# Optimization experiments

Measured on AMD Instinct MI355X. Metric: run time of the kernel, lower is better.

## Reference

```python
import jax, jax.numpy as jnp
import numpy as np

N, E, D, F = 8192, 262144, 256, 512  # nodes, edges, hidden_dim, ffn hidden
M = 256  # performer num_random_features (default)


def _ln(x, g, b, eps=1e-5):
    mu = jnp.mean(x, axis=-1, keepdims=True)
    var = jnp.mean((x - mu) ** 2, axis=-1, keepdims=True)
    return (x - mu) * jax.lax.rsqrt(var + eps) * g + b


def setup_inputs() -> dict:
    key = jax.random.key(0)
    ks = jax.random.split(key, 16)
    s = 1.0 / np.sqrt(D)
    return {
        "h": jax.random.normal(ks[0], (N, D), dtype=jnp.float32),
        "edge_index": jax.random.randint(ks[1], (2, E), 0, N, dtype=jnp.int32),
        "W_gcn": jax.random.normal(ks[2], (D, D), dtype=jnp.float32) * s,
        "b_gcn": jnp.zeros((D,), jnp.float32),
        "Wq": jax.random.normal(ks[3], (D, D), dtype=jnp.float32) * s,
        "bq": jnp.zeros((D,), jnp.float32),
        "Wk": jax.random.normal(ks[4], (D, D), dtype=jnp.float32) * s,
        "bk": jnp.zeros((D,), jnp.float32),
        "Wv": jax.random.normal(ks[5], (D, D), dtype=jnp.float32) * s,
        "bv": jnp.zeros((D,), jnp.float32),
        "Wo": jax.random.normal(ks[6], (D, D), dtype=jnp.float32) * s,
        "bo": jnp.zeros((D,), jnp.float32),
        "RF": jax.random.normal(ks[7], (M, D), dtype=jnp.float32) * s,  # random feature projection
        "g1": jnp.ones((D,), jnp.float32), "be1": jnp.zeros((D,), jnp.float32),
        "g2": jnp.ones((D,), jnp.float32), "be2": jnp.zeros((D,), jnp.float32),
        "g3": jnp.ones((D,), jnp.float32), "be3": jnp.zeros((D,), jnp.float32),
        "W1": jax.random.normal(ks[8], (D, F), dtype=jnp.float32) * s,
        "b1": jnp.zeros((F,), jnp.float32),
        "W2": jax.random.normal(ks[9], (F, D), dtype=jnp.float32) * (1.0 / np.sqrt(F)),
        "b2": jnp.zeros((D,), jnp.float32),
    }


def _gps_forward(h, edge_index, W_gcn, b_gcn, Wq, bq, Wk, bk, Wv, bv, Wo, bo, RF,
                 g1, be1, g2, be2, g3, be3, W1, b1, W2, b2):
    n = h.shape[0]
    # ---- local GCNConv (add self loops, symmetric norm) ----
    loops = jnp.arange(n, dtype=edge_index.dtype)
    src = jnp.concatenate([edge_index[0], loops])
    dst = jnp.concatenate([edge_index[1], loops])
    deg = jax.ops.segment_sum(jnp.ones_like(src, dtype=h.dtype), dst, num_segments=n)
    dinv = jnp.where(deg > 0, jax.lax.rsqrt(jnp.maximum(deg, 1e-12)), 0.0)
    coef = dinv[src] * dinv[dst]  # [E+N]
    xw = h @ W_gcn  # [N, D]
    h_local = jax.ops.segment_sum(xw[src] * coef[:, None], dst, num_segments=n) + b_gcn
    h1 = _ln(h + h_local, g1, be1)  # dropout p applied in train only; eval here
    # ---- global Performer attention (as written: dense NxN in feature space) ----
    q = h1 @ Wq + bq
    k = h1 @ Wk + bk
    v = h1 @ Wv + bv
    qf = q @ RF.T  # [N, M]
    kf = k @ RF.T  # [N, M]
    scores = (qf @ kf.T) / jnp.sqrt(jnp.asarray(h.shape[-1], h.dtype))  # [N, N]
    attw = jax.nn.softmax(scores, axis=-1)
    h_global = (attw @ v) @ Wo + bo
    h2 = _ln(h1 + h_global, g2, be2)
    # ---- FFN ----
    h_ffn = jnp.maximum(h2 @ W1 + b1, 0.0) @ W2 + b2
    return _ln(h2 + h_ffn, g3, be3)


def reference(h, edge_index, W_gcn, b_gcn, Wq, bq, Wk, bk, Wv, bv, Wo, bo, RF,
              g1, be1, g2, be2, g3, be3, W1, b1, W2, b2):
    return _gps_forward(h, edge_index, W_gcn, b_gcn, Wq, bq, Wk, bk, Wv, bv, Wo, bo, RF,
                        g1, be1, g2, be2, g3, be3, W1, b1, W2, b2)
```

## Files before the change

### kernel.cpp

```cpp
#include <hip/hip_runtime.h>
#include <hip/hip_bf16.h>

#define NN 8192
#define EE 262144
#define DD 256
#define FF 512
#define MM 256

typedef __attribute__((ext_vector_type(8))) short short8v;
typedef __attribute__((ext_vector_type(16))) float float16v;

__device__ __forceinline__ ushort f2bf(float x) {
  union { float f; unsigned u; } c; c.f = x;
  unsigned r = (c.u + 0x7FFF + ((c.u >> 16) & 1)) >> 16;
  return (ushort)r;
}
__device__ __forceinline__ float b2f(ushort u) {
  union { unsigned u; float f; } c; c.u = ((unsigned)u) << 16;
  return c.f;
}
__device__ __forceinline__ void async_copy16(void* lds, const void* g) {
  __builtin_amdgcn_global_load_lds(
      (const __attribute__((address_space(1))) void*)g,
      (__attribute__((address_space(3))) void*)lds, 16, 0, 0);
}

__global__ void count_kernel(const int* __restrict__ ei, int* __restrict__ degi) {
  int i = blockIdx.x * blockDim.x + threadIdx.x;
  if (i < EE) atomicAdd(&degi[ei[EE + i]], 1);
}

__global__ __launch_bounds__(1024) void scan_kernel(const int* __restrict__ degi,
                                                    int* __restrict__ csr_off,
                                                    float* __restrict__ dinv) {
  __shared__ int part[1024];
  int tid = threadIdx.x;
  int base = tid * 8;
  int loc[8], dv[8]; int s = 0;
#pragma unroll
  for (int i = 0; i < 8; ++i) { int d = degi[base + i]; dv[i] = d; loc[i] = s; s += d; }
  part[tid] = s;
  __syncthreads();
  for (int off = 1; off < 1024; off <<= 1) {
    int v = (tid >= off) ? part[tid - off] : 0;
    __syncthreads();
    part[tid] += v;
    __syncthreads();
  }
  int pre = (tid == 0) ? 0 : part[tid - 1];
#pragma unroll
  for (int i = 0; i < 8; ++i) {
    csr_off[base + i] = pre + loc[i];
    dinv[base + i] = rsqrtf((float)(dv[i] + 1));
  }
  if (tid == 1023) csr_off[NN] = part[1023];
}

__global__ void fill_kernel(const int* __restrict__ ei, const int* __restrict__ csr_off,
                            int* __restrict__ cursor, int* __restrict__ csr_src) {
  int i = blockIdx.x * blockDim.x + threadIdx.x;
  if (i < EE) {
    int d = ei[EE + i];
    int pos = csr_off[d] + atomicAdd(&cursor[d], 1);
    csr_src[pos] = ei[i];
  }
}

#define QSCALE 0.090168441f
#define P1B 10753
__global__ __launch_bounds__(256) void prep_kernel(
    const float* __restrict__ h, const float* __restrict__ W_gcn,
    const float* __restrict__ Wv, const float* __restrict__ Wo,
    const float* __restrict__ W1, const float* __restrict__ W2,
    const float* __restrict__ bv,
    const float* __restrict__ Wq, const float* __restrict__ Wk,
    const float* __restrict__ bq, const float* __restrict__ bk,
    const float* __restrict__ RF,
    ushort* __restrict__ hb, ushort* __restrict__ WgcnT, ushort* __restrict__ Wcat,
    ushort* __restrict__ WoT, ushort* __restrict__ W1T, ushort* __restrict__ W2T,
    ushort* __restrict__ RFb, ushort* __restrict__ Wqb, ushort* __restrict__ Wkb,
    float* __restrict__ bcat, int* __restrict__ degi, int* __restrict__ cursor)
{
  if (blockIdx.x < P1B) {
    int i = blockIdx.x * 256 + threadIdx.x;
    const int R0 = NN * DD;
    const int R1 = R0 + DD * DD;
    const int R2 = R1 + DD * DD;
    const int R3 = R2 + DD * DD;
    const int R4 = R3 + DD * FF;
    const int R5 = R4 + FF * DD;
    const int R6 = R5 + DD;
    const int R7 = R6 + DD * DD;
    const int R8 = R7 + DD * DD;
    const int R9 = R8 + DD * DD;
    if (i < R0) {
      hb[i] = f2bf(h[i]);
    } else if (i < R1) {
      int j = i - R0; int n = j >> 8, k = j & 255;
      WgcnT[(n << 8) | k] = f2bf(W_gcn[k * DD + n]);
    } else if (i < R2) {
      int j = i - R1; int n = j >> 8, k = j & 255;
      Wcat[((512 + n) << 8) | k] = f2bf(Wv[k * DD + n]);
    } else if (i < R3) {
      int j = i - R2; int n = j >> 8, k = j & 255;
      WoT[(n << 8) | k] = f2bf(Wo[k * DD + n]);
    } else if (i < R4) {
      int j = i - R3; int n = j >> 8, k = j & 255;
      W1T[(n << 8) | k] = f2bf(W1[k * FF + n]);
    } else if (i < R5) {
      int j = i - R4; int n = j >> 9, k = j & 511;
      W2T[n * FF + k] = f2bf(W2[k * DD + n]);
    } else if (i < R6) {
      bcat[512 + (i - R5)] = bv[i - R5];
    } else if (i < R7) {
      int j = i - R6;
      RFb[j] = f2bf(RF[j]);
    } else if (i < R8) {
      int j = i - R7;
      Wqb[j] = f2bf(Wq[j] * QSCALE);
    } else if (i < R9) {
      int j = i - R8;
      Wkb[j] = f2bf(Wk[j]);
    }
  } else if (blockIdx.x < P1B + 2) {
    const int b = blockIdx.x - P1B;
    const int m = threadIdx.x;
    const float* bvec = (b == 0) ? bq : bk;
    const float alpha = (b == 0) ? QSCALE : 1.0f;
    float s = 0.0f;
    for (int j = 0; j < DD; ++j) s = fmaf(bvec[j], RF[m * DD + j], s);
    bcat[(b == 0 ? 0 : 256) + m] = s * alpha;
  } else {
    int i = (blockIdx.x - P1B - 2) * 256 + threadIdx.x;
    if (i < NN) { degi[i] = 0; cursor[i] = 0; }
  }
}

template<int OMODE, bool RELU>
__global__ __launch_bounds__(512) void gemm_bf16_kernel(
    const ushort* __restrict__ A, const ushort* __restrict__ BT,
    const float* __restrict__ bias, void* __restrict__ Cv,
    void* __restrict__ Cv2, void* __restrict__ Cv3,
    int M, int N, int K)
{
  __shared__ ushort As[2][4096];
  __shared__ ushort Bs[2][4096];
  const int tid = threadIdx.x;
  const int c32 = tid & 31, hi = (tid >> 5) & 1;
  const int wv = tid >> 6;
  const int q = wv & 3, ks = wv >> 2;
  const int qm = (q >> 1) << 5, qn = (q & 1) << 5;
  const int m0 = blockIdx.y * 64, n0 = blockIdx.x * 64;

  const int sr = tid >> 3, spsl = tid & 7;
  const int ssl = spsl ^ ((sr >> 2) & 7);
  const ushort* Asrc = A + (size_t)(m0 + sr) * K + (ssl << 3);
  const ushort* Bsrc = BT + (size_t)(n0 + sr) * K + (ssl << 3);

  const int ra = qm + c32, rb = qn + c32;
  const int ga = (ra >> 2) & 7, gb = (rb >> 2) & 7;

  float16v acc = (float16v)(0.0f);

#define GS(b, k0) { \
    async_copy16(&As[b][tid << 3], Asrc + (k0)); \
    async_copy16(&Bs[b][tid << 3], Bsrc + (k0)); }

  GS(0, 0)
  const int nk = K >> 6;
  for (int kt = 0; kt < nk; ++kt) {
    asm volatile("s_waitcnt vmcnt(0)" ::: "memory");
    __syncthreads();
    if (kt + 1 < nk) GS((kt + 1) & 1, (kt + 1) << 6)
    const ushort* as_ = As[kt & 1];
    const ushort* bs_ = Bs[kt & 1];
    __builtin_amdgcn_s_setprio(1);
#pragma unroll
    for (int k2 = 0; k2 < 2; ++k2) {
      const int k16 = (ks << 1) + k2;
      const int sl = (k16 << 1) + hi;
      short8v af = *(const short8v*)&as_[(ra << 6) + ((sl ^ ga) << 3)];
      short8v bf = *(const short8v*)&bs_[(rb << 6) + ((sl ^ gb) << 3)];
      acc = __builtin_amdgcn_mfma_f32_32x32x16_bf16(af, bf, acc, 0, 0, 0);
    }
    __builtin_amdgcn_s_setprio(0);
  }
#undef GS

  __syncthreads();
  float* red = (float*)&As[0][0];
  if (ks == 1) {
#pragma unroll
    for (int r = 0; r < 16; ++r) {
      const int crow = (r & 3) + ((r >> 2) << 3) + (hi << 2);
      red[(q << 10) + (crow << 5) + c32] = acc[r];
    }
  }
  __syncthreads();
  if (ks == 0) {
    const int col = n0 + qn + c32;
    const float bv = bias ? bias[col] : 0.0f;
#pragma unroll
    for (int r = 0; r < 16; ++r) {
      const int crow = (r & 3) + ((r >> 2) << 3) + (hi << 2);
      const int m = m0 + qm + crow;
      float v = acc[r] + red[(q << 10) + (crow << 5) + c32] + bv;
      if (RELU) v = fmaxf(v, 0.0f);
      if (OMODE == 0) {
        ((float*)Cv)[(size_t)m * N + col] = v;
      } else if (OMODE == 4) {
        ((ushort*)Cv)[(size_t)m * N + col] = f2bf(v);
      } else {
        if (col < 256) {
          ((ushort*)Cv)[(size_t)m * 256 + col] = f2bf(v);
        } else if (col < 512) {
          const int c2 = (col - 256) ^ ((m & 7) << 3) ^ (((m >> 3) & 3) << 6);
          ((ushort*)Cv2)[(size_t)m * 256 + c2] = f2bf(v);
        } else {
          ((ushort*)Cv3)[(size_t)(col - 512) * NN + m] = f2bf(v);
        }
      }
    }
  }
}

__global__ __launch_bounds__(256) void gcn_gather_ln_kernel(
    const ushort* __restrict__ xwb, const float* __restrict__ h,
    const float* __restrict__ dinv, const int* __restrict__ csr_off,
    const int* __restrict__ csr_src, const float* __restrict__ b_gcn,
    const float* __restrict__ g1, const float* __restrict__ be1,
    float* __restrict__ h1, ushort* __restrict__ h1b)
{
  const int node = blockIdx.x * 4 + (threadIdx.x >> 6);
  const int t = threadIdx.x & 63;
  const int c4 = t << 2;
  const float di = dinv[node];
  const int e0 = csr_off[node], e1 = csr_off[node + 1];
  float acc[4] = {0.f, 0.f, 0.f, 0.f};
  for (int e = e0; e < e1; ++e) {
    int s = csr_src[e];
    float ds = dinv[s];
    ushort4 xv = *(const ushort4*)&xwb[(size_t)s * DD + c4];
    acc[0] = fmaf(b2f(xv.x), ds, acc[0]);
    acc[1] = fmaf(b2f(xv.y), ds, acc[1]);
    acc[2] = fmaf(b2f(xv.z), ds, acc[2]);
    acc[3] = fmaf(b2f(xv.w), ds, acc[3]);
  }
  ushort4 sv = *(const ushort4*)&xwb[(size_t)node * DD + c4];
  float4 hv = *(const float4*)&h[(size_t)node * DD + c4];
  float4 bg = *(const float4*)&b_gcn[c4];
  const float dii = di * di;
  float y[4];
  y[0] = fmaf(acc[0], di, b2f(sv.x) * dii) + bg.x + hv.x;
  y[1] = fmaf(acc[1], di, b2f(sv.y) * dii) + bg.y + hv.y;
  y[2] = fmaf(acc[2], di, b2f(sv.z) * dii) + bg.z + hv.z;
  y[3] = fmaf(acc[3], di, b2f(sv.w) * dii) + bg.w + hv.w;
  float s1 = (y[0] + y[1]) + (y[2] + y[3]);
  float s2 = (y[0]*y[0] + y[1]*y[1]) + (y[2]*y[2] + y[3]*y[3]);
#pragma unroll
  for (int m = 1; m <= 32; m <<= 1) { s1 += __shfl_xor(s1, m); s2 += __shfl_xor(s2, m); }
  float mu = s1 * (1.0f / 256.0f);
  float var = s2 * (1.0f / 256.0f) - mu * mu;
  float inv = rsqrtf(fmaxf(var, 0.0f) + 1e-5f);
  float4 g4 = *(const float4*)&g1[c4];
  float4 b4 = *(const float4*)&be1[c4];
  float v0 = (y[0] - mu) * inv * g4.x + b4.x;
  float v1 = (y[1] - mu) * inv * g4.y + b4.y;
  float v2 = (y[2] - mu) * inv * g4.z + b4.z;
  float v3 = (y[3] - mu) * inv * g4.w + b4.w;
  *(float4*)&h1[(size_t)node * DD + c4] = make_float4(v0, v1, v2, v3);
  ushort4 ob; ob.x = f2bf(v0); ob.y = f2bf(v1); ob.z = f2bf(v2); ob.w = f2bf(v3);
  *(ushort4*)&h1b[(node << 8) + c4] = ob;
}

__global__ __launch_bounds__(256) void ln_res_kernel(
    const float* __restrict__ a, const float* __restrict__ b,
    const float* __restrict__ g, const float* __restrict__ be,
    float* __restrict__ out, ushort* __restrict__ outb)
{
  const int row = blockIdx.x * 4 + (threadIdx.x >> 6);
  const int t = threadIdx.x & 63;
  const int c4 = t << 2;
  float4 av = *(const float4*)&a[(size_t)row * DD + c4];
  float4 bv = *(const float4*)&b[(size_t)row * DD + c4];
  float y[4] = {av.x + bv.x, av.y + bv.y, av.z + bv.z, av.w + bv.w};
  float s1 = (y[0] + y[1]) + (y[2] + y[3]);
  float s2 = (y[0]*y[0] + y[1]*y[1]) + (y[2]*y[2] + y[3]*y[3]);
#pragma unroll
  for (int m = 1; m <= 32; m <<= 1) { s1 += __shfl_xor(s1, m); s2 += __shfl_xor(s2, m); }
  float mu = s1 * (1.0f / 256.0f);
  float var = s2 * (1.0f / 256.0f) - mu * mu;
  float inv = rsqrtf(fmaxf(var, 0.0f) + 1e-5f);
  float4 g4 = *(const float4*)&g[c4];
  float4 b4 = *(const float4*)&be[c4];
  float v0 = (y[0] - mu) * inv * g4.x + b4.x;
  float v1 = (y[1] - mu) * inv * g4.y + b4.y;
  float v2 = (y[2] - mu) * inv * g4.z + b4.z;
  float v3 = (y[3] - mu) * inv * g4.w + b4.w;
  *(float4*)&out[(size_t)row * DD + c4] = make_float4(v0, v1, v2, v3);
  if (outb) {
    ushort4 ob; ob.x = f2bf(v0); ob.y = f2bf(v1); ob.z = f2bf(v2); ob.w = f2bf(v3);
    *(ushort4*)&outb[(row << 8) + c4] = ob;
  }
}

__global__ __launch_bounds__(256, 2) void flash_mfma_kernel(
    const ushort* __restrict__ qb, const ushort* __restrict__ kb,
    const ushort* __restrict__ vbT, ushort* __restrict__ opb,
    float* __restrict__ ml, int ksn, int kchunk)
{
  __shared__ ushort Kbuf[2][8192];
  __shared__ ushort Vbuf[2][8192];

  const int tid = threadIdx.x;
  const int l = tid & 63, wv = tid >> 6;
  const int c32 = l & 31, hi = l >> 5;
  const int qt = blockIdx.x / ksn, ks = blockIdx.x % ksn;
  const int q0 = qt * 128;
  const int kbase = ks * kchunk;

  const int vrow = tid >> 2;
  const ushort* kptr = kb + (size_t)(kbase + (tid >> 5)) * 256 + ((tid & 31) << 3);
  const ushort* vptr = vbT + (size_t)vrow * NN + kbase + (((tid & 3) ^ ((vrow >> 3) & 3)) << 3);

#define FSTAGE(b) { \
    _Pragma("unroll") \
    for (int c = 0; c < 4; ++c) { \
      async_copy16(&Kbuf[b][((c << 8) + tid) << 3], kptr + (size_t)c * (8 * 256)); \
      async_copy16(&Vbuf[b][((c << 8) + tid) << 3], vptr + (size_t)c * (64 * NN)); \
    } }

  FSTAGE(0)

  short8v qfr[16];
  {
    const ushort* qrow = qb + (size_t)(q0 + wv * 32 + c32) * 256 + (hi << 3);
#pragma unroll
    for (int kk = 0; kk < 16; ++kk)
      qfr[kk] = *(const short8v*)(qrow + (kk << 4));
  }

  float16v acc[8];
#pragma unroll
  for (int dt = 0; dt < 8; ++dt) acc[dt] = (float16v)(0.0f);
  float lsum = 0.f;

  const int ksw = ((c32 & 7) << 3) | (((c32 >> 3) & 3) << 6);
  const int vsw = (c32 >> 3) & 3;
  const int voff0 = (hi ^ vsw) << 3;
  const int voff1 = ((2 + hi) ^ vsw) << 3;

  const int nit = kchunk >> 5;
  for (int it = 0; it < nit; ++it) {
    asm volatile("s_waitcnt vmcnt(0)" ::: "memory");
    __syncthreads();
    if (it + 1 < nit) {
      kptr += 32 * 256;
      vptr += 32;
      FSTAGE((it + 1) & 1)
    }
    const ushort* Kp = Kbuf[it & 1];
    const ushort* Vp = Vbuf[it & 1];

    float16v s = (float16v)(0.0f);
    __builtin_amdgcn_s_setprio(1);
#pragma unroll
    for (int kk = 0; kk < 16; ++kk) {
      short8v kf = *(const short8v*)&Kp[(c32 << 8) + (((kk << 4) + (hi << 3)) ^ ksw)];
      s = __builtin_amdgcn_mfma_f32_32x32x16_bf16(kf, qfr[kk], s, 0, 0, 0);
    }
    __builtin_amdgcn_s_setprio(0);

    float p[16];
#pragma unroll
    for (int r = 0; r < 16; ++r) p[r] = exp2f(s[r]);
    {
      float t0 = (p[0] + p[1]) + (p[2] + p[3]);
      float t1 = (p[4] + p[5]) + (p[6] + p[7]);
      float t2 = (p[8] + p[9]) + (p[10] + p[11]);
      float t3 = (p[12] + p[13]) + (p[14] + p[15]);
      lsum += (t0 + t1) + (t2 + t3);
    }
    unsigned u0, u1, u2, u3, u4, u5, u6, u7;
    asm("v_cvt_pk_bf16_f32 %0, %1, %2" : "=v"(u0) : "v"(p[0]),  "v"(p[1]));
    asm("v_cvt_pk_bf16_f32 %0, %1, %2" : "=v"(u1) : "v"(p[2]),  "v"(p[3]));
    asm("v_cvt_pk_bf16_f32 %0, %1, %2" : "=v"(u2) : "v"(p[4]),  "v"(p[5]));
    asm("v_cvt_pk_bf16_f32 %0, %1, %2" : "=v"(u3) : "v"(p[6]),  "v"(p[7]));
    asm("v_cvt_pk_bf16_f32 %0, %1, %2" : "=v"(u4) : "v"(p[8]),  "v"(p[9]));
    asm("v_cvt_pk_bf16_f32 %0, %1, %2" : "=v"(u5) : "v"(p[10]), "v"(p[11]));
    asm("v_cvt_pk_bf16_f32 %0, %1, %2" : "=v"(u6) : "v"(p[12]), "v"(p[13]));
    asm("v_cvt_pk_bf16_f32 %0, %1, %2" : "=v"(u7) : "v"(p[14]), "v"(p[15]));
    asm volatile("v_permlane32_swap_b32 %0, %1" : "+v"(u0), "+v"(u2));
    asm volatile("v_permlane32_swap_b32 %0, %1" : "+v"(u1), "+v"(u3));
    asm volatile("v_permlane32_swap_b32 %0, %1" : "+v"(u4), "+v"(u6));
    asm volatile("v_permlane32_swap_b32 %0, %1" : "+v"(u5), "+v"(u7));
    union { unsigned uu[4]; short8v v; } P0, P1;
    P0.uu[0] = u0; P0.uu[1] = u1; P0.uu[2] = u2; P0.uu[3] = u3;
    P1.uu[0] = u4; P1.uu[1] = u5; P1.uu[2] = u6; P1.uu[3] = u7;

    __builtin_amdgcn_s_setprio(1);
#pragma unroll
    for (int dt = 0; dt < 8; ++dt) {
      const int drow = (dt << 5) + c32;
      short8v vf0 = *(const short8v*)&Vp[(drow << 5) + voff0];
      short8v vf1 = *(const short8v*)&Vp[(drow << 5) + voff1];
      acc[dt] = __builtin_amdgcn_mfma_f32_32x32x16_bf16(P0.v, vf0, acc[dt], 0, 0, 0);
      acc[dt] = __builtin_amdgcn_mfma_f32_32x32x16_bf16(P1.v, vf1, acc[dt], 0, 0, 0);
    }
    __builtin_amdgcn_s_setprio(0);
  }
#undef FSTAGE

  float lt = lsum + __shfl_xor(lsum, 32);
  if (hi == 0) ml[(size_t)ks * NN + q0 + wv * 32 + c32] = lt;
  ushort* op = opb + (size_t)ks * (NN * DD);
#pragma unroll
  for (int dt = 0; dt < 8; ++dt)
#pragma unroll
    for (int r = 0; r < 16; ++r) {
      const int qrow = q0 + wv * 32 + (r & 3) + ((r >> 2) << 3) + (hi << 2);
      op[(size_t)qrow * DD + (dt << 5) + c32] = f2bf(acc[dt][r]);
    }
}

__global__ __launch_bounds__(256) void flash_merge_kernel(
    const ushort* __restrict__ opb, const float* __restrict__ ml,
    ushort* __restrict__ hgb, int ksn)
{
  const int t = threadIdx.x;
  const int row = blockIdx.x * 8 + (t >> 5);
  const int cg = t & 31;
  float num[8] = {0.f, 0.f, 0.f, 0.f, 0.f, 0.f, 0.f, 0.f};
  float L = 0.f;
  for (int i = 0; i < ksn; ++i) {
    L += ml[(size_t)i * NN + row];
    short8v v = *(const short8v*)&opb[(size_t)i * NN * DD + (size_t)row * DD + (cg << 3)];
#pragma unroll
    for (int j = 0; j < 8; ++j) num[j] += b2f((ushort)v[j]);
  }
  float inv = 1.0f / L;
  short8v o;
#pragma unroll
  for (int j = 0; j < 8; ++j) o[j] = (short)f2bf(num[j] * inv);
  *(short8v*)&hgb[(row << 8) + (cg << 3)] = o;
}

extern "C" void kernel_launch(void* const* d_in, const int* in_sizes, int n_in,
                              void* d_out, int out_size, void* d_ws, size_t ws_size,
                              hipStream_t stream) {
  (void)in_sizes; (void)n_in; (void)out_size;
  const float* h     = (const float*)d_in[0];
  const int*   ei    = (const int*)  d_in[1];
  const float* W_gcn = (const float*)d_in[2];
  const float* b_gcn = (const float*)d_in[3];
  const float* Wq    = (const float*)d_in[4];
  const float* bq    = (const float*)d_in[5];
  const float* Wk    = (const float*)d_in[6];
  const float* bk    = (const float*)d_in[7];
  const float* Wv    = (const float*)d_in[8];
  const float* bv    = (const float*)d_in[9];
  const float* Wo    = (const float*)d_in[10];
  const float* bo    = (const float*)d_in[11];
  const float* RF    = (const float*)d_in[12];
  const float* g1    = (const float*)d_in[13];
  const float* be1   = (const float*)d_in[14];
  const float* g2    = (const float*)d_in[15];
  const float* be2   = (const float*)d_in[16];
  const float* g3    = (const float*)d_in[17];
  const float* be3   = (const float*)d_in[18];
  const float* W1    = (const float*)d_in[19];
  const float* b1    = (const float*)d_in[20];
  const float* W2    = (const float*)d_in[21];
  const float* b2    = (const float*)d_in[22];
  float* out = (float*)d_out;

  const size_t M2 = (size_t)NN * DD;
  const int ksn = (ws_size >= (size_t)64 * 1024 * 1024) ? 8 : 4;
  const int kchunk = NN / ksn;

  char* base = (char*)d_ws;
  float*  h1   = (float*)base;  base += M2 * 4;
  ushort* hbX  = (ushort*)base; base += M2 * 2;
  ushort* h1bX = (ushort*)base; base += M2 * 2;
  ushort* qb   = (ushort*)base; base += M2 * 2;
  ushort* kb   = (ushort*)base; base += M2 * 2;
  ushort* vbT  = (ushort*)base; base += M2 * 2;
  ushort* opb  = (ushort*)base;
  float*  R    = (float*)opb;   base += (size_t)ksn * M2 * 2;
  float*  mlf  = (float*)base;  base += (size_t)8 * NN * 4;
  ushort* WgcnT = (ushort*)base; base += DD * DD * 2;
  ushort* Wcat  = (ushort*)base; base += (size_t)768 * DD * 2;
  ushort* WoT   = (ushort*)base; base += DD * DD * 2;
  ushort* W1T   = (ushort*)base; base += FF * DD * 2;
  ushort* W2T   = (ushort*)base; base += DD * FF * 2;
  ushort* RFb   = (ushort*)base; base += DD * DD * 2;
  ushort* Wqb   = (ushort*)base; base += DD * DD * 2;
  ushort* Wkb   = (ushort*)base; base += DD * DD * 2;
  float*  bcat  = (float*)base;  base += 768 * 4;
  float*  dinv  = (float*)base;  base += NN * 4;
  int* degi    = (int*)base; base += NN * 4;
  int* cursor  = (int*)base; base += NN * 4;
  int* csr_off = (int*)base; base += (NN + 4) * 4;
  int* csr_src = (int*)base; base += EE * 4;

  ushort* xwb = (ushort*)R;
  float*  hgo = R;
  float*  h2  = R + M2;
  ushort* tb  = qb;
  float*  f2  = h1;
  ushort* hgb = hbX;
  ushort* h2b = h1bX;

  prep_kernel<<<P1B + 2 + 32, 256, 0, stream>>>(
      h, W_gcn, Wv, Wo, W1, W2, bv, Wq, Wk, bq, bk, RF,
      hbX, WgcnT, Wcat, WoT, W1T, W2T, RFb, Wqb, Wkb, bcat, degi, cursor);

  gemm_bf16_kernel<4, false><<<dim3(4, 4), 512, 0, stream>>>(
      RFb, Wqb, nullptr, Wcat, nullptr, nullptr, DD, DD, DD);
  gemm_bf16_kernel<4, false><<<dim3(4, 4), 512, 0, stream>>>(
      RFb, Wkb, nullptr, Wcat + 256 * 256, nullptr, nullptr, DD, DD, DD);

  count_kernel<<<EE / 256, 256, 0, stream>>>(ei, degi);
  scan_kernel<<<1, 1024, 0, stream>>>(degi, csr_off, dinv);
  fill_kernel<<<EE / 256, 256, 0, stream>>>(ei, csr_off, cursor, csr_src);

  gemm_bf16_kernel<4, false><<<dim3(DD / 64, NN / 64), 512, 0, stream>>>(
      hbX, WgcnT, nullptr, xwb, nullptr, nullptr, NN, DD, DD);
  gcn_gather_ln_kernel<<<NN / 4, 256, 0, stream>>>(xwb, h, dinv, csr_off, csr_src, b_gcn, g1, be1, h1, h1bX);
  gemm_bf16_kernel<3, false><<<dim3(768 / 64, NN / 64), 512, 0, stream>>>(
      h1bX, Wcat, bcat, qb, kb, vbT, NN, 768, DD);
  flash_mfma_kernel<<<(NN / 128) * ksn, 256, 0, stream>>>(qb, kb, vbT, opb, mlf, ksn, kchunk);
  flash_merge_kernel<<<NN / 8, 256, 0, stream>>>(opb, mlf, hgb, ksn);
  gemm_bf16_kernel<0, false><<<dim3(DD / 64, NN / 64), 512, 0, stream>>>(
      hgb, WoT, bo, hgo, nullptr, nullptr, NN, DD, DD);
  ln_res_kernel<<<NN / 4, 256, 0, stream>>>(h1, hgo, g2, be2, h2, h2b);
  gemm_bf16_kernel<4, true ><<<dim3(FF / 64, NN / 64), 512, 0, stream>>>(
      h2b, W1T, b1, tb, nullptr, nullptr, NN, FF, DD);
  gemm_bf16_kernel<0, false><<<dim3(DD / 64, NN / 64), 512, 0, stream>>>(
      tb, W2T, b2, f2, nullptr, nullptr, NN, DD, FF);
  ln_res_kernel<<<NN / 4, 256, 0, stream>>>(h2, f2, g3, be3, out, nullptr);
}
```

Baseline: 225.9 us.

## Fuse output projection, LayerNorms and FFN into one epilogue kernel; merge prep launches

Replaces the Wo GEMM, two residual LayerNorm kernels and both FFN GEMMs with a single per-32-row kernel that keeps h2 and the ReLU intermediate in LDS. This removes several global round trips of NxD and NxF activations and four launches. It also folds the degree counting into prep_kernel, merges the two RF·Wq/Wk GEMMs into one launch, and vectorises the transposed V store. The cost is that the fused kernel uses a lot of LDS per block and reads weights directly from global memory without staging them.

After: 215.6 us. 1.05x faster.

```diff
diff --git a/kernel.cpp b/kernel.cpp
--- a/kernel.cpp
+++ b/kernel.cpp
@@ -23,11 +23,6 @@
   __builtin_amdgcn_global_load_lds(
       (const __attribute__((address_space(1))) void*)g,
       (__attribute__((address_space(3))) void*)lds, 16, 0, 0);
-}
-
-__global__ void count_kernel(const int* __restrict__ ei, int* __restrict__ degi) {
-  int i = blockIdx.x * blockDim.x + threadIdx.x;
-  if (i < EE) atomicAdd(&degi[ei[EE + i]], 1);
 }
 
 __global__ __launch_bounds__(1024) void scan_kernel(const int* __restrict__ degi,
@@ -75,11 +70,11 @@
     const float* __restrict__ bv,
     const float* __restrict__ Wq, const float* __restrict__ Wk,
     const float* __restrict__ bq, const float* __restrict__ bk,
-    const float* __restrict__ RF,
+    const float* __restrict__ RF, const int* __restrict__ ei,
     ushort* __restrict__ hb, ushort* __restrict__ WgcnT, ushort* __restrict__ Wcat,
     ushort* __restrict__ WoT, ushort* __restrict__ W1T, ushort* __restrict__ W2T,
-    ushort* __restrict__ RFb, ushort* __restrict__ Wqb, ushort* __restrict__ Wkb,
-    float* __restrict__ bcat, int* __restrict__ degi, int* __restrict__ cursor)
+    ushort* __restrict__ RFb, ushort* __restrict__ Wqkb,
+    float* __restrict__ bcat, int* __restrict__ degi)
 {
   if (blockIdx.x < P1B) {
     int i = blockIdx.x * 256 + threadIdx.x;
@@ -117,10 +112,10 @@
       RFb[j] = f2bf(RF[j]);
     } else if (i < R8) {
       int j = i - R7;
-      Wqb[j] = f2bf(Wq[j] * QSCALE);
+      Wqkb[j] = f2bf(Wq[j] * QSCALE);
     } else if (i < R9) {
       int j = i - R8;
-      Wkb[j] = f2bf(Wk[j]);
+      Wqkb[DD * DD + j] = f2bf(Wk[j]);
     }
   } else if (blockIdx.x < P1B + 2) {
     const int b = blockIdx.x - P1B;
@@ -132,7 +127,7 @@
     bcat[(b == 0 ? 0 : 256) + m] = s * alpha;
   } else {
     int i = (blockIdx.x - P1B - 2) * 256 + threadIdx.x;
-    if (i < NN) { degi[i] = 0; cursor[i] = 0; }
+    if (i < EE) atomicAdd(&degi[ei[EE + i]], 1);
   }
 }
 
@@ -200,24 +195,35 @@
   if (ks == 0) {
     const int col = n0 + qn + c32;
     const float bv = bias ? bias[col] : 0.0f;
-#pragma unroll
-    for (int r = 0; r < 16; ++r) {
-      const int crow = (r & 3) + ((r >> 2) << 3) + (hi << 2);
-      const int m = m0 + qm + crow;
-      float v = acc[r] + red[(q << 10) + (crow << 5) + c32] + bv;
-      if (RELU) v = fmaxf(v, 0.0f);
-      if (OMODE == 0) {
-        ((float*)Cv)[(size_t)m * N + col] = v;
-      } else if (OMODE == 4) {
-        ((ushort*)Cv)[(size_t)m * N + col] = f2bf(v);
-      } else {
-        if (col < 256) {
-          ((ushort*)Cv)[(size_t)m * 256 + col] = f2bf(v);
-        } else if (col < 512) {
-          const int c2 = (col - 256) ^ ((m & 7) << 3) ^ (((m >> 3) & 3) << 6);
-          ((ushort*)Cv2)[(size_t)m * 256 + c2] = f2bf(v);
+    if (OMODE == 3 && col >= 512) {
+#pragma unroll
+      for (int g = 0; g < 4; ++g) {
+        float v0 = acc[g * 4 + 0] + red[(q << 10) + (((0) + (g << 3) + (hi << 2)) << 5) + c32] + bv;
+        float v1 = acc[g * 4 + 1] + red[(q << 10) + (((1) + (g << 3) + (hi << 2)) << 5) + c32] + bv;
+        float v2 = acc[g * 4 + 2] + red[(q << 10) + (((2) + (g << 3) + (hi << 2)) << 5) + c32] + bv;
+        float v3 = acc[g * 4 + 3] + red[(q << 10) + (((3) + (g << 3) + (hi << 2)) << 5) + c32] + bv;
+        ushort4 o; o.x = f2bf(v0); o.y = f2bf(v1); o.z = f2bf(v2); o.w = f2bf(v3);
+        *(ushort4*)&((ushort*)Cv3)[(size_t)(col - 512) * NN + m0 + qm + (g << 3) + (hi << 2)] = o;
+      }
+    } else {
+#pragma unroll
+      for (int r = 0; r < 16; ++r) {
+        const int crow = (r & 3) + ((r >> 2) << 3) + (hi << 2);
+        const int m = m0 + qm + crow;
+        float v = acc[r] + red[(q << 10) + (crow << 5) + c32] + bv;
+        if (RELU) v = fmaxf(v, 0.0f);
+        if (OMODE == 4) {
+          ((ushort*)Cv)[(size_t)m * N + col] = f2bf(v);
+        } else if (OMODE == 5) {
+          if (col < 256) ((ushort*)Cv)[(size_t)m * 256 + col] = f2bf(v);
+          else ((ushort*)Cv)[(size_t)(256 + m) * 256 + (col - 256)] = f2bf(v);
         } else {
-          ((ushort*)Cv3)[(size_t)(col - 512) * NN + m] = f2bf(v);
+          if (col < 256) {
+            ((ushort*)Cv)[(size_t)m * 256 + col] = f2bf(v);
+          } else {
+            const int c2 = (col - 256) ^ ((m & 7) << 3) ^ (((m >> 3) & 3) << 6);
+            ((ushort*)Cv2)[(size_t)m * 256 + c2] = f2bf(v);
+          }
         }
       }
     }
@@ -273,37 +279,6 @@
   *(ushort4*)&h1b[(node << 8) + c4] = ob;
 }
 
-__global__ __launch_bounds__(256) void ln_res_kernel(
-    const float* __restrict__ a, const float* __restrict__ b,
-    const float* __restrict__ g, const float* __restrict__ be,
-    float* __restrict__ out, ushort* __restrict__ outb)
-{
-  const int row = blockIdx.x * 4 + (threadIdx.x >> 6);
-  const int t = threadIdx.x & 63;
-  const int c4 = t << 2;
-  float4 av = *(const float4*)&a[(size_t)row * DD + c4];
-  float4 bv = *(const float4*)&b[(size_t)row * DD + c4];
-  float y[4] = {av.x + bv.x, av.y + bv.y, av.z + bv.z, av.w + bv.w};
-  float s1 = (y[0] + y[1]) + (y[2] + y[3]);
-  float s2 = (y[0]*y[0] + y[1]*y[1]) + (y[2]*y[2] + y[3]*y[3]);
-#pragma unroll
-  for (int m = 1; m <= 32; m <<= 1) { s1 += __shfl_xor(s1, m); s2 += __shfl_xor(s2, m); }
-  float mu = s1 * (1.0f / 256.0f);
-  float var = s2 * (1.0f / 256.0f) - mu * mu;
-  float inv = rsqrtf(fmaxf(var, 0.0f) + 1e-5f);
-  float4 g4 = *(const float4*)&g[c4];
-  float4 b4 = *(const float4*)&be[c4];
-  float v0 = (y[0] - mu) * inv * g4.x + b4.x;
-  float v1 = (y[1] - mu) * inv * g4.y + b4.y;
-  float v2 = (y[2] - mu) * inv * g4.z + b4.z;
-  float v3 = (y[3] - mu) * inv * g4.w + b4.w;
-  *(float4*)&out[(size_t)row * DD + c4] = make_float4(v0, v1, v2, v3);
-  if (outb) {
-    ushort4 ob; ob.x = f2bf(v0); ob.y = f2bf(v1); ob.z = f2bf(v2); ob.w = f2bf(v3);
-    *(ushort4*)&outb[(row << 8) + c4] = ob;
-  }
-}
-
 __global__ __launch_bounds__(256, 2) void flash_mfma_kernel(
     const ushort* __restrict__ qb, const ushort* __restrict__ kb,
     const ushort* __restrict__ vbT, ushort* __restrict__ opb,
@@ -443,6 +418,146 @@
 #pragma unroll
   for (int j = 0; j < 8; ++j) o[j] = (short)f2bf(num[j] * inv);
   *(short8v*)&hgb[(row << 8) + (cg << 3)] = o;
+}
+
+__global__ __launch_bounds__(512, 4) void epilogue_kernel(
+    const ushort* __restrict__ hgb, const float* __restrict__ h1,
+    const ushort* __restrict__ WoT, const float* __restrict__ bo,
+    const float* __restrict__ g2, const float* __restrict__ be2,
+    const ushort* __restrict__ W1T, const float* __restrict__ b1,
+    const ushort* __restrict__ W2T, const float* __restrict__ b2,
+    const float* __restrict__ g3, const float* __restrict__ be3,
+    float* __restrict__ out)
+{
+  __shared__ float  yL[32 * 256];
+  __shared__ ushort h2bL[32 * 256];
+  __shared__ ushort tL[32 * 512];
+
+  const int tid = threadIdx.x;
+  const int c32 = tid & 31, hi = (tid >> 5) & 1;
+  const int wv = tid >> 6;
+  const int lane = tid & 63;
+  const int m0 = blockIdx.x * 32;
+  const int n0 = wv << 5;
+  const int col = n0 + c32;
+
+  float16v acc = (float16v)(0.0f);
+#pragma unroll
+  for (int k0 = 0; k0 < 256; k0 += 16) {
+    short8v af = *(const short8v*)&hgb[(size_t)(m0 + c32) * 256 + k0 + (hi << 3)];
+    short8v bf = *(const short8v*)&WoT[(size_t)col * 256 + k0 + (hi << 3)];
+    acc = __builtin_amdgcn_mfma_f32_32x32x16_bf16(af, bf, acc, 0, 0, 0);
+  }
+  {
+    const float bov = bo[col];
+#pragma unroll
+    for (int r = 0; r < 16; ++r) {
+      const int row = (r & 3) + ((r >> 2) << 3) + (hi << 2);
+      yL[(row << 8) + col] = acc[r] + bov + h1[(size_t)(m0 + row) * 256 + col];
+    }
+  }
+  __syncthreads();
+#pragma unroll
+  for (int rr = 0; rr < 4; ++rr) {
+    const int row = (wv << 2) + rr;
+    const int c4 = lane << 2;
+    float4 v = *(const float4*)&yL[(row << 8) + c4];
+    float s1 = (v.x + v.y) + (v.z + v.w);
+    float s2 = (v.x * v.x + v.y * v.y) + (v.z * v.z + v.w * v.w);
+#pragma unroll
+    for (int m = 1; m <= 32; m <<= 1) { s1 += __shfl_xor(s1, m); s2 += __shfl_xor(s2, m); }
+    float mu = s1 * (1.0f / 256.0f);
+    float var = s2 * (1.0f / 256.0f) - mu * mu;
+    float inv = rsqrtf(fmaxf(var, 0.0f) + 1e-5f);
+    float4 g4 = *(const float4*)&g2[c4];
+    float4 b4 = *(const float4*)&be2[c4];
+    float o0 = (v.x - mu) * inv * g4.x + b4.x;
+    float o1 = (v.y - mu) * inv * g4.y + b4.y;
+    float o2 = (v.z - mu) * inv * g4.z + b4.z;
+    float o3 = (v.w - mu) * inv * g4.w + b4.w;
+    *(float4*)&yL[(row << 8) + c4] = make_float4(o0, o1, o2, o3);
+    const int psl = (c4 >> 3) ^ (row & 7);
+    ushort4 ob; ob.x = f2bf(o0); ob.y = f2bf(o1); ob.z = f2bf(o2); ob.w = f2bf(o3);
+    *(ushort4*)&h2bL[(row << 8) + (psl << 3) + (c4 & 7)] = ob;
+  }
+  __syncthreads();
+  {
+    float16v a1[2] = {(float16v)(0.0f), (float16v)(0.0f)};
+    const int f0 = wv << 6;
+#pragma unroll
+    for (int k0 = 0; k0 < 256; k0 += 16) {
+      const int s = (k0 >> 3) + hi;
+      short8v af = *(const short8v*)&h2bL[(c32 << 8) + ((s ^ (c32 & 7)) << 3)];
+#pragma unroll
+      for (int nt = 0; nt < 2; ++nt) {
+        short8v bf = *(const short8v*)&W1T[(size_t)(f0 + (nt << 5) + c32) * 256 + k0 + (hi << 3)];
+        a1[nt] = __builtin_amdgcn_mfma_f32_32x32x16_bf16(af, bf, a1[nt], 0, 0, 0);
+      }
+    }
+#pragma unroll
+    for (int nt = 0; nt < 2; ++nt) {
+      const int col1 = f0 + (nt << 5) + c32;
+      const float b1v = b1[col1];
+#pragma unroll
+      for (int r = 0; r < 16; ++r) {
+        const int row = (r & 3) + ((r >> 2) << 3) + (hi << 2);
+        float v = fmaxf(a1[nt][r] + b1v, 0.0f);
+        const int psl = (col1 >> 3) ^ (row & 7);
+        tL[(row << 9) + (psl << 3) + (col1 & 7)] = f2bf(v);
+      }
+    }
+  }
+  __syncthreads();
+  float16v a2 = (float16v)(0.0f);
+#pragma unroll
+  for (int k0 = 0; k0 < 512; k0 += 16) {
+    const int s = (k0 >> 3) + hi;
+    short8v af = *(const short8v*)&tL[(c32 << 9) + ((s ^ (c32 & 7)) << 3)];
+    short8v bf = *(const short8v*)&W2T[(size_t)col * 512 + k0 + (hi << 3)];
+    a2 = __builtin_amdgcn_mfma_f32_32x32x16_bf16(af, bf, a2, 0, 0, 0);
+  }
+  {
+    const float b2v = b2[col];
+#pragma unroll
+    for (int r = 0; r < 16; ++r) {
+      const int row = (r & 3) + ((r >> 2) << 3) + (hi << 2);
+      a2[r] += b2v + yL[(row << 8) + col];
+    }
+  }
+  __syncthreads();
+  {
+    float* y2L = (float*)tL;
+#pragma unroll
+    for (int r = 0; r < 16; ++r) {
+      const int row = (r & 3) + ((r >> 2) << 3) + (hi << 2);
+      y2L[(row << 8) + col] = a2[r];
+    }
+  }
+  __syncthreads();
+  {
+    const float* y2L = (const float*)tL;
+#pragma unroll
+    for (int rr = 0; rr < 4; ++rr) {
+      const int row = (wv << 2) + rr;
+      const int c4 = lane << 2;
+      float4 v = *(const float4*)&y2L[(row << 8) + c4];
+      float s1 = (v.x + v.y) + (v.z + v.w);
+      float s2 = (v.x * v.x + v.y * v.y) + (v.z * v.z + v.w * v.w);
+#pragma unroll
+      for (int m = 1; m <= 32; m <<= 1) { s1 += __shfl_xor(s1, m); s2 += __shfl_xor(s2, m); }
+      float mu = s1 * (1.0f / 256.0f);
+      float var = s2 * (1.0f / 256.0f) - mu * mu;
+      float inv = rsqrtf(fmaxf(var, 0.0f) + 1e-5f);
+      float4 g4 = *(const float4*)&g3[c4];
+      float4 b4 = *(const float4*)&be3[c4];
+      float4 o;
+      o.x = (v.x - mu) * inv * g4.x + b4.x;
+      o.y = (v.y - mu) * inv * g4.y + b4.y;
+      o.z = (v.z - mu) * inv * g4.z + b4.z;
+      o.w = (v.w - mu) * inv * g4.w + b4.w;
+      *(float4*)&out[(size_t)(m0 + row) * 256 + c4] = o;
+    }
+  }
 }
 
 extern "C" void kernel_launch(void* const* d_in, const int* in_sizes, int n_in,
@@ -494,8 +609,7 @@
   ushort* W1T   = (ushort*)base; base += FF * DD * 2;
   ushort* W2T   = (ushort*)base; base += DD * FF * 2;
   ushort* RFb   = (ushort*)base; base += DD * DD * 2;
-  ushort* Wqb   = (ushort*)base; base += DD * DD * 2;
-  ushort* Wkb   = (ushort*)base; base += DD * DD * 2;
+  ushort* Wqkb  = (ushort*)base; base += (size_t)2 * DD * DD * 2;
   float*  bcat  = (float*)base;  base += 768 * 4;
   float*  dinv  = (float*)base;  base += NN * 4;
   int* degi    = (int*)base; base += NN * 4;
@@ -504,25 +618,19 @@
   int* csr_src = (int*)base; base += EE * 4;
 
   ushort* xwb = (ushort*)R;
-  float*  hgo = R;
-  float*  h2  = R + M2;
-  ushort* tb  = qb;
-  float*  f2  = h1;
   ushort* hgb = hbX;
-  ushort* h2b = h1bX;
-
-  prep_kernel<<<P1B + 2 + 32, 256, 0, stream>>>(
-      h, W_gcn, Wv, Wo, W1, W2, bv, Wq, Wk, bq, bk, RF,
-      hbX, WgcnT, Wcat, WoT, W1T, W2T, RFb, Wqb, Wkb, bcat, degi, cursor);
-
-  gemm_bf16_kernel<4, false><<<dim3(4, 4), 512, 0, stream>>>(
-      RFb, Wqb, nullptr, Wcat, nullptr, nullptr, DD, DD, DD);
-  gemm_bf16_kernel<4, false><<<dim3(4, 4), 512, 0, stream>>>(
-      RFb, Wkb, nullptr, Wcat + 256 * 256, nullptr, nullptr, DD, DD, DD);
-
-  count_kernel<<<EE / 256, 256, 0, stream>>>(ei, degi);
+
+  hipMemsetAsync(degi, 0, (size_t)2 * NN * sizeof(int), stream);
+
+  prep_kernel<<<P1B + 2 + 1024, 256, 0, stream>>>(
+      h, W_gcn, Wv, Wo, W1, W2, bv, Wq, Wk, bq, bk, RF, ei,
+      hbX, WgcnT, Wcat, WoT, W1T, W2T, RFb, Wqkb, bcat, degi);
+
   scan_kernel<<<1, 1024, 0, stream>>>(degi, csr_off, dinv);
   fill_kernel<<<EE / 256, 256, 0, stream>>>(ei, csr_off, cursor, csr_src);
+
+  gemm_bf16_kernel<5, false><<<dim3(8, 4), 512, 0, stream>>>(
+      RFb, Wqkb, nullptr, Wcat, nullptr, nullptr, DD, 512, DD);
 
   gemm_bf16_kernel<4, false><<<dim3(DD / 64, NN / 64), 512, 0, stream>>>(
       hbX, WgcnT, nullptr, xwb, nullptr, nullptr, NN, DD, DD);
@@ -531,12 +639,6 @@
       h1bX, Wcat, bcat, qb, kb, vbT, NN, 768, DD);
   flash_mfma_kernel<<<(NN / 128) * ksn, 256, 0, stream>>>(qb, kb, vbT, opb, mlf, ksn, kchunk);
   flash_merge_kernel<<<NN / 8, 256, 0, stream>>>(opb, mlf, hgb, ksn);
-  gemm_bf16_kernel<0, false><<<dim3(DD / 64, NN / 64), 512, 0, stream>>>(
-      hgb, WoT, bo, hgo, nullptr, nullptr, NN, DD, DD);
-  ln_res_kernel<<<NN / 4, 256, 0, stream>>>(h1, hgo, g2, be2, h2, h2b);
-  gemm_bf16_kernel<4, true ><<<dim3(FF / 64, NN / 64), 512, 0, stream>>>(
-      h2b, W1T, b1, tb, nullptr, nullptr, NN, FF, DD);
-  gemm_bf16_kernel<0, false><<<dim3(DD / 64, NN / 64), 512, 0, stream>>>(
-      tb, W2T, b2, f2, nullptr, nullptr, NN, DD, FF);
-  ln_res_kernel<<<NN / 4, 256, 0, stream>>>(h2, f2, g3, be3, out, nullptr);
-}
+  epilogue_kernel<<<NN / 32, 512, 0, stream>>>(
+      hgb, h1, WoT, bo, g2, be2, W1T, b1, W2T, b2, g3, be3, out);
+}
```
